# Kernel tuning notes

Hardware: AMD Instinct MI355X
Metric: run time of the kernel (lower is better)

Reference implementation:

```python
import jax, jax.numpy as jnp
import numpy as np

N, E, G = 50000, 500000, 1024
ND, ED, H, L, OUT = 32, 16, 128, 4, 1
BN_EPS = 1e-5


def setup_inputs() -> dict:
    key = jax.random.key(0)
    ks = jax.random.split(key, 32)

    def w(k, shape, fan):
        return jax.random.normal(k, shape, jnp.float32) / np.float32(np.sqrt(fan))

    inp = {
        "x": jax.random.normal(ks[0], (N, ND), jnp.float32),
        "edge_index": jax.random.randint(ks[1], (2, E), 0, N, jnp.int64),
        "edge_attr": jax.random.normal(ks[2], (E, ED), jnp.float32),
        "batch": jax.random.randint(ks[3], (N,), 0, G, jnp.int64),
        # embeddings
        "ne_w": w(ks[4], (ND, H), ND), "ne_b": jnp.zeros((H,), jnp.float32),
        "ee_w": w(ks[5], (ED, H), ED), "ee_b": jnp.zeros((H,), jnp.float32),
        # per-layer node_mlp: Linear(2H,H) ReLU Linear(H,H) BN(H)
        "nm_w1": w(ks[6], (L, 2 * H, H), 2 * H), "nm_b1": jnp.zeros((L, H), jnp.float32),
        "nm_w2": w(ks[7], (L, H, H), H), "nm_b2": jnp.zeros((L, H), jnp.float32),
        "bn_g": jnp.ones((L, H), jnp.float32), "bn_b": jnp.zeros((L, H), jnp.float32),
        # per-layer edge_mlp: Linear(H,H) ReLU Linear(H,H)  (edge_dim==hidden_dim inside MPNN)
        "em_w1": w(ks[8], (L, H, H), H), "em_b1": jnp.zeros((L, H), jnp.float32),
        "em_w2": w(ks[9], (L, H, H), H), "em_b2": jnp.zeros((L, H), jnp.float32),
        # readout: Linear(H,H) ReLU Dropout(eval=identity) Linear(H,OUT)
        "ro_w1": w(ks[10], (H, H), H), "ro_b1": jnp.zeros((H,), jnp.float32),
        "ro_w2": w(ks[11], (H, OUT), H), "ro_b2": jnp.zeros((OUT,), jnp.float32),
    }
    return inp


def reference(x, edge_index, edge_attr, batch,
              ne_w, ne_b, ee_w, ee_b,
              nm_w1, nm_b1, nm_w2, nm_b2, bn_g, bn_b,
              em_w1, em_b1, em_w2, em_b2,
              ro_w1, ro_b1, ro_w2, ro_b2):
    src, dst = edge_index[0], edge_index[1]  # PyG default: x_j from source, aggregate at target
    h = x @ ne_w + ne_b                      # [N, H]
    e = edge_attr @ ee_w + ee_b              # [E, H]
    inv_std = np.float32(1.0 / np.sqrt(1.0 + BN_EPS))  # eval BN, running_mean=0, running_var=1
    for l in range(nm_w1.shape[0]):
        # edge_mlp
        e = jax.nn.relu(e @ em_w1[l] + em_b1[l]) @ em_w2[l] + em_b2[l]
        # message: concat(x_j, edge_attr) -> node_mlp
        msg = jnp.concatenate([h[src], e], axis=1)              # [E, 2H]
        msg = jax.nn.relu(msg @ nm_w1[l] + nm_b1[l]) @ nm_w2[l] + nm_b2[l]
        msg = msg * (inv_std * bn_g[l]) + bn_b[l]               # BatchNorm1d (eval)
        # scatter-add aggregation + residual update
        agg = jax.ops.segment_sum(msg, dst, num_segments=h.shape[0])
        h = agg + h
    pooled = jax.ops.segment_sum(h, batch, num_segments=G)      # global_add_pool -> [G, H]
    return jax.nn.relu(pooled @ ro_w1 + ro_b1) @ ro_w2 + ro_b2  # [G, OUT]
```

## Files before the change

### kernel.cpp

```cpp
#include <hip/hip_runtime.h>
#include <hip/hip_bf16.h>
#include <math.h>

#define NN 50000
#define EE 500000
#define GG 1024
#define NDIM 32
#define EDIM 16
#define HH 128
#define LL 4
#define NT2 ((EE + 127) / 128)
#define NB2 ((NN + 127) / 128)
#define SCAN_NB ((NN + 255) / 256)

typedef unsigned short ushortT;
typedef __attribute__((ext_vector_type(8))) short bf16x8;
typedef __attribute__((ext_vector_type(4))) float f32x4;

#define MFMA16(a, b, c) __builtin_amdgcn_mfma_f32_16x16x32_bf16(a, b, c, 0, 0, 0)

__device__ inline float bf2f(ushortT u) {
    union { unsigned int i; float f; } v; v.i = ((unsigned int)u) << 16; return v.f;
}
__device__ inline ushortT f2bf(float f) {
    union { float f; unsigned int i; } v; v.f = f;
    unsigned int r = v.i + 0x7FFFu + ((v.i >> 16) & 1u);
    return (ushortT)(r >> 16);
}
__device__ inline short f2bfs(float f) { return (short)f2bf(f); }

__device__ inline bf16x8 lds_a(const char* base, int strideB, int row, int colByte,
                               int mask) {
    int b = row * strideB + colByte;
    b ^= ((row & mask) << 4);
    return *reinterpret_cast<const bf16x8*>(base + b);
}

__global__ __launch_bounds__(256) void hist_kernel(
        const int* __restrict__ dst, int* __restrict__ counts) {
    int i = blockIdx.x * 256 + threadIdx.x;
    if (i < EE) atomicAdd(&counts[dst[i]], 1);
}

__global__ __launch_bounds__(256) void scan_part1(
        const int* __restrict__ counts, int* __restrict__ bsum) {
    __shared__ int buf[256];
    int t = threadIdx.x;
    int i = blockIdx.x * 256 + t;
    buf[t] = (i < NN) ? counts[i] : 0;
    __syncthreads();
    for (int s = 128; s > 0; s >>= 1) {
        if (t < s) buf[t] += buf[t + s];
        __syncthreads();
    }
    if (t == 0) bsum[blockIdx.x] = buf[0];
}

__global__ __launch_bounds__(256) void scan_part2(
        const int* __restrict__ bsum, int* __restrict__ bbase) {
    __shared__ int buf[256];
    int t = threadIdx.x;
    int v = (t < SCAN_NB) ? bsum[t] : 0;
    buf[t] = v;
    __syncthreads();
    for (int off = 1; off < 256; off <<= 1) {
        int s = (t >= off) ? buf[t - off] : 0;
        __syncthreads();
        buf[t] += s;
        __syncthreads();
    }
    if (t < SCAN_NB) bbase[t] = buf[t] - v;
}

__global__ __launch_bounds__(256) void scan_part3(
        const int* __restrict__ counts, const int* __restrict__ bbase,
        int* __restrict__ base) {
    __shared__ int buf[256];
    int t = threadIdx.x;
    int i = blockIdx.x * 256 + t;
    int v = (i < NN) ? counts[i] : 0;
    buf[t] = v;
    __syncthreads();
    for (int off = 1; off < 256; off <<= 1) {
        int s = (t >= off) ? buf[t - off] : 0;
        __syncthreads();
        buf[t] += s;
        __syncthreads();
    }
    if (i < NN) base[i] = bbase[blockIdx.x] + buf[t] - v;
}

__global__ __launch_bounds__(256) void build_perm_kernel(
        const int* __restrict__ src, const int* __restrict__ dst,
        const int* __restrict__ base, int* __restrict__ cnt,
        int* __restrict__ perm, int* __restrict__ srcS, int* __restrict__ dstS) {
    int i = blockIdx.x * 256 + threadIdx.x;
    if (i >= EE) return;
    int d = dst[i];
    int pos = base[d] + atomicAdd(&cnt[d], 1);
    perm[pos] = i;
    srcS[pos] = src[i];
    dstS[pos] = d;
}

__global__ __launch_bounds__(256) void transpose_kernel(
        const float* __restrict__ in, ushortT* __restrict__ out, int K, int N) {
    int per = K * N;
    int total = LL * per;
    int idx = blockIdx.x * 256 + threadIdx.x;
    if (idx >= total) return;
    int l = idx / per, rem = idx - l * per;
    int n = rem / K, k = rem - n * K;
    out[idx] = f2bf(in[(size_t)l * per + (size_t)k * N + n]);
}

__global__ __launch_bounds__(256) void transpose_ee_kernel(
        const float* __restrict__ in, ushortT* __restrict__ out) {
    int idx = blockIdx.x * 256 + threadIdx.x;
    if (idx >= HH * 32) return;
    int n = idx >> 5, k = idx & 31;
    out[idx] = (k < EDIM) ? f2bf(in[k * HH + n]) : (ushortT)0;
}

__global__ __launch_bounds__(256) void bnfold_kernel(
        const float* __restrict__ w2, const float* __restrict__ b2,
        const float* __restrict__ bng, const float* __restrict__ bnb,
        ushortT* __restrict__ w2g, float* __restrict__ nb2g, float inv_std) {
    int idx = blockIdx.x * 256 + threadIdx.x;
    if (idx < LL * HH * HH) {
        int l = idx / (HH * HH), rem = idx - l * (HH * HH);
        int n = rem / HH, k = rem - n * HH;
        w2g[idx] = f2bf(w2[(size_t)l * HH * HH + (size_t)k * HH + n] *
                        bng[l * HH + n] * inv_std);
    }
    if (idx < LL * HH) {
        nb2g[idx] = b2[idx] * bng[idx] * inv_std + bnb[idx];
    }
}

__global__ __launch_bounds__(128) void node_embed_kernel(
        const float* __restrict__ x, const float* __restrict__ w,
        const float* __restrict__ b, float* __restrict__ h) {
    __shared__ float xs[NDIM];
    int i = blockIdx.x, j = threadIdx.x;
    if (j < NDIM) xs[j] = x[(size_t)i * NDIM + j];
    __syncthreads();
    float acc = b[j];
#pragma unroll
    for (int k = 0; k < NDIM; ++k) acc += xs[k] * w[k * HH + j];
    h[(size_t)i * HH + j] = acc;
}

template<int K, int KS, bool HASB>
__device__ inline void gemm_b(const char* aBase, int aStrideB, int aMask,
        const ushortT* __restrict__ wT, const float* __restrict__ bias,
        int wr, int wc, int l15, int lg, f32x4 acc[2][4]) {
#pragma unroll
    for (int ntl = 0; ntl < 4; ++ntl) {
        float bb = HASB ? bias[wc * 64 + ntl * 16 + l15] : 0.f;
        f32x4 iv = {bb, bb, bb, bb};
        acc[0][ntl] = iv;
        acc[1][ntl] = iv;
    }
#pragma unroll
    for (int ks = 0; ks < K / 32; ++ks) {
        int kk = ks * 32 + lg * 8;
        bf16x8 a0 = lds_a(aBase, aStrideB, wr * 32 + l15,      kk * 2, aMask);
        bf16x8 a1 = lds_a(aBase, aStrideB, wr * 32 + 16 + l15, kk * 2, aMask);
#pragma unroll
        for (int ntl = 0; ntl < 4; ++ntl) {
            int n = wc * 64 + ntl * 16 + l15;
            bf16x8 b = *reinterpret_cast<const bf16x8*>(wT + (size_t)n * KS + kk);
            acc[0][ntl] = MFMA16(a0, b, acc[0][ntl]);
            acc[1][ntl] = MFMA16(a1, b, acc[1][ntl]);
        }
    }
}

__device__ inline void gemm_uinit3(const char* aBase, const char* uBase,
        const ushortT* __restrict__ wT,
        int wr, int wc, int l15, int lg, f32x4 acc[2][4]) {
#pragma unroll
    for (int mt = 0; mt < 2; ++mt)
#pragma unroll
        for (int ntl = 0; ntl < 4; ++ntl) {
            int col = wc * 64 + ntl * 16 + l15;
#pragma unroll
            for (int r = 0; r < 4; ++r) {
                int row = wr * 32 + mt * 16 + lg * 4 + r;
                int b = row * 256 + col * 2; b ^= ((row & 7) << 4);
                acc[mt][ntl][r] = bf2f(*reinterpret_cast<const ushortT*>(uBase + b));
            }
        }
#pragma unroll
    for (int ks = 0; ks < 4; ++ks) {
        int kk = ks * 32 + lg * 8;
        bf16x8 a0 = lds_a(aBase, 256, wr * 32 + l15,      kk * 2, 7);
        bf16x8 a1 = lds_a(aBase, 256, wr * 32 + 16 + l15, kk * 2, 7);
#pragma unroll
        for (int ntl = 0; ntl < 4; ++ntl) {
            int n = wc * 64 + ntl * 16 + l15;
            bf16x8 b = *reinterpret_cast<const bf16x8*>(wT + (size_t)n * 256 + kk);
            acc[0][ntl] = MFMA16(a0, b, acc[0][ntl]);
            acc[1][ntl] = MFMA16(a1, b, acc[1][ntl]);
        }
    }
}

__device__ inline void wfrag(char* base, int wr, int wc, int l15, int lg,
                             f32x4 acc[2][4], bool relu) {
#pragma unroll
    for (int mt = 0; mt < 2; ++mt)
#pragma unroll
        for (int ntl = 0; ntl < 4; ++ntl) {
            int col = wc * 64 + ntl * 16 + l15;
#pragma unroll
            for (int r = 0; r < 4; ++r) {
                int row = wr * 32 + mt * 16 + lg * 4 + r;
                int b = row * 256 + col * 2;
                b ^= ((row & 7) << 4);
                float v = acc[mt][ntl][r];
                if (relu) v = fmaxf(v, 0.f);
                *reinterpret_cast<ushortT*>(base + b) = f2bf(v);
            }
        }
}

template<int EMBED, int LASTL>
__global__ __launch_bounds__(512) void edgeA_kernel(
        const ushortT* __restrict__ u, ushortT* __restrict__ e,
        const int* __restrict__ srcS, const int* __restrict__ dstS,
        const int* __restrict__ basep, const int* __restrict__ perm,
        const float* __restrict__ ea,
        const ushortT* __restrict__ eewT, const float* __restrict__ eeb,
        const ushortT* __restrict__ ew1t, const float* __restrict__ eb1,
        const ushortT* __restrict__ ew2t, const float* __restrict__ eb2,
        const ushortT* __restrict__ nw1bt,
        ushortT* __restrict__ partials) {
    __shared__ __align__(16) char eT[128 * 256];
    __shared__ __align__(16) char uT[128 * 256];
    __shared__ int dstx[128], bstartL[128], sidx[128], pidx[128];

    const int e0 = blockIdx.x * 128;
    int V = EE - e0; if (V > 128) V = 128;
    const int tid = threadIdx.x;
    const bf16x8 z8 = {0, 0, 0, 0, 0, 0, 0, 0};

    if (tid < 128) {
        int ii = e0 + tid;
        int d = (ii < EE) ? dstS[ii] : -1;
        dstx[tid] = d;
        bstartL[tid] = (d >= 0) ? basep[d] : 0;
        sidx[tid] = (ii < EE) ? srcS[ii] : 0;
        if (EMBED) pidx[tid] = (ii < EE) ? perm[ii] : 0;
    }
    __syncthreads();

#pragma unroll
    for (int s = 0; s < 4; ++s) {
        int idx = tid + s * 512;
        int row = idx >> 4, c8 = (idx & 15) * 8;
        bf16x8 v = *reinterpret_cast<const bf16x8*>(u + (size_t)sidx[row] * HH + c8);
        int b = row * 256 + c8 * 2; b ^= ((row & 7) << 4);
        *reinterpret_cast<bf16x8*>(uT + b) = v;
    }
    if (EMBED) {
        {
            int row = tid >> 2, q4 = (tid & 3) * 4;
            float4 v = *reinterpret_cast<const float4*>(
                ea + (size_t)pidx[row] * EDIM + q4);
            unsigned long long pack =
                (unsigned long long)f2bf(v.x) |
                ((unsigned long long)f2bf(v.y) << 16) |
                ((unsigned long long)f2bf(v.z) << 32) |
                ((unsigned long long)f2bf(v.w) << 48);
            int b = row * 64 + q4 * 2; b ^= ((row & 3) << 4);
            *reinterpret_cast<unsigned long long*>(eT + b) = pack;
        }
        if (tid < 256) {
            int row = tid >> 1;
            int b = row * 64 + 32 + (tid & 1) * 16; b ^= ((row & 3) << 4);
            *reinterpret_cast<bf16x8*>(eT + b) = z8;
        }
    } else {
#pragma unroll
        for (int s = 0; s < 4; ++s) {
            int idx = tid + s * 512;
            int row = idx >> 4, c8 = (idx & 15) * 8;
            bf16x8 v = *reinterpret_cast<const bf16x8*>(
                e + (size_t)(e0 + row) * HH + c8);
            int b = row * 256 + c8 * 2; b ^= ((row & 7) << 4);
            *reinterpret_cast<bf16x8*>(eT + b) = v;
        }
    }
    __syncthreads();

    const int wid = tid >> 6, lane = tid & 63;
    const int wr = wid >> 1, wc = wid & 1, l15 = lane & 15, lg = lane >> 4;
    f32x4 acc[2][4];

    if (EMBED) {
        gemm_b<32, 32, true>(eT, 64, 3, eewT, eeb, wr, wc, l15, lg, acc);
        __syncthreads();
        wfrag(eT, wr, wc, l15, lg, acc, false);
        __syncthreads();
    }
    gemm_b<HH, HH, true>(eT, 256, 7, ew1t, eb1, wr, wc, l15, lg, acc);
    __syncthreads();
    wfrag(eT, wr, wc, l15, lg, acc, true);
    __syncthreads();
    gemm_b<HH, HH, true>(eT, 256, 7, ew2t, eb2, wr, wc, l15, lg, acc);
    __syncthreads();
    wfrag(eT, wr, wc, l15, lg, acc, false);
    __syncthreads();
    if (!LASTL) {
#pragma unroll
        for (int s = 0; s < 4; ++s) {
            int idx = tid + s * 512;
            int row = idx >> 4, c8 = (idx & 15) * 8;
            if (row < V) {
                int b = row * 256 + c8 * 2; b ^= ((row & 7) << 4);
                *reinterpret_cast<bf16x8*>(e + (size_t)(e0 + row) * HH + c8) =
                    *reinterpret_cast<const bf16x8*>(eT + b);
            }
        }
    }
    gemm_uinit3(eT, uT, nw1bt, wr, wc, l15, lg, acc);
    __syncthreads();
    wfrag(eT, wr, wc, l15, lg, acc, true);
    __syncthreads();

    {
        int col = tid & 127, seg = tid >> 7;
        int r = seg * 32, rend = r + 32;
        float sum = 0.f;
        int dprev = -1, runStart = r;
        for (; r < rend; ++r) {
            int d = dstx[r];
            if (d != dprev) {
                if (dprev >= 0) {
                    int slot = ((e0 + runStart) >> 5) - (bstartL[runStart] >> 5);
                    if (slot < 3)
                        partials[((size_t)slot * NN + dprev) * HH + col] = f2bf(sum);
                }
                sum = 0.f; dprev = d; runStart = r;
            }
            if (d >= 0) {
                int b = r * 256 + col * 2; b ^= ((r & 7) << 4);
                sum += bf2f(*reinterpret_cast<const ushortT*>(eT + b));
            }
        }
        if (dprev >= 0) {
            int slot = ((e0 + runStart) >> 5) - (bstartL[runStart] >> 5);
            if (slot < 3)
                partials[((size_t)slot * NN + dprev) * HH + col] = f2bf(sum);
        }
    }
}

template<int HASU>
__global__ __launch_bounds__(512) void nodeB_kernel(
        const ushortT* __restrict__ partials, const int* __restrict__ basep,
        const ushortT* __restrict__ w2g, const float* __restrict__ nb2g,
        float* __restrict__ h,
        const ushortT* __restrict__ w1tn, const float* __restrict__ b1n,
        ushortT* __restrict__ uOut) {
    __shared__ __align__(16) char sT[128 * 256];
    __shared__ int degx[128];
    const int n0 = blockIdx.x * 128;
    int V = NN - n0; if (V > 128) V = 128;
    const int tid = threadIdx.x;

    __shared__ int basex[128];
    if (tid < 128) {
        int bs = 0, de = 0;
        if (tid < V) {
            int n = n0 + tid;
            bs = basep[n];
            int be = (n + 1 < NN) ? basep[n + 1] : EE;
            de = be - bs;
        }
        basex[tid] = bs;
        degx[tid] = de;
    }
    __syncthreads();

#pragma unroll
    for (int g = 0; g < 4; ++g) {
        int node = g * 32 + (tid >> 4);
        int c8 = (tid & 15) * 8;
        float s[8] = {0.f, 0.f, 0.f, 0.f, 0.f, 0.f, 0.f, 0.f};
        if (node < V) {
            int bs = basex[node], de = degx[node];
            if (de > 0) {
                int ns = ((bs + de - 1) >> 5) - (bs >> 5) + 1;
                if (ns > 3) ns = 3;
                for (int sl = 0; sl < ns; ++sl) {
                    bf16x8 pv = *reinterpret_cast<const bf16x8*>(
                        partials + ((size_t)sl * NN + n0 + node) * HH + c8);
#pragma unroll
                    for (int j = 0; j < 8; ++j) s[j] += bf2f((ushortT)pv[j]);
                }
            }
        }
        bf16x8 o;
#pragma unroll
        for (int j = 0; j < 8; ++j) o[j] = f2bfs(s[j]);
        int b = node * 256 + c8 * 2; b ^= ((node & 7) << 4);
        *reinterpret_cast<bf16x8*>(sT + b) = o;
    }
    __syncthreads();

    const int wid = tid >> 6, lane = tid & 63;
    const int wr = wid >> 1, wc = wid & 1, l15 = lane & 15, lg = lane >> 4;
    f32x4 acc[2][4];

    gemm_b<HH, HH, false>(sT, 256, 7, w2g, nullptr, wr, wc, l15, lg, acc);
#pragma unroll
    for (int ntl = 0; ntl < 4; ++ntl) {
        int col = wc * 64 + ntl * 16 + l15;
        float bg = nb2g[col];
#pragma unroll
        for (int mt = 0; mt < 2; ++mt)
#pragma unroll
            for (int r = 0; r < 4; ++r) {
                int row = wr * 32 + mt * 16 + lg * 4 + r;
                if (row < V) {
                    size_t off = (size_t)(n0 + row) * HH + col;
                    float hn = h[off] + acc[mt][ntl][r] + (float)degx[row] * bg;
                    h[off] = hn;
                    acc[mt][ntl][r] = hn;
                } else {
                    acc[mt][ntl][r] = 0.f;
                }
            }
    }
    if (HASU) {
        __syncthreads();
        wfrag(sT, wr, wc, l15, lg, acc, false);
        __syncthreads();
        gemm_b<HH, 2 * HH, true>(sT, 256, 7, w1tn, b1n, wr, wc, l15, lg, acc);
        __syncthreads();
        wfrag(sT, wr, wc, l15, lg, acc, false);
        __syncthreads();
#pragma unroll
        for (int s = 0; s < 4; ++s) {
            int idx = tid + s * 512;
            int row = idx >> 4, c8 = (idx & 15) * 8;
            if (row < V) {
                int b = row * 256 + c8 * 2; b ^= ((row & 7) << 4);
                *reinterpret_cast<bf16x8*>(uOut + (size_t)(n0 + row) * HH + c8) =
                    *reinterpret_cast<const bf16x8*>(sT + b);
            }
        }
    }
}

__global__ __launch_bounds__(512) void node_pre_kernel(
        const float* __restrict__ h, const ushortT* __restrict__ w1t,
        const float* __restrict__ b1, ushortT* __restrict__ uo) {
    __shared__ __align__(16) char sT[128 * 256];
    const int n0 = blockIdx.x * 128;
    int V = NN - n0; if (V > 128) V = 128;
    const int tid = threadIdx.x;
#pragma unroll
    for (int s = 0; s < 4; ++s) {
        int idx = tid + s * 512;
        int row = idx >> 4, c8 = (idx & 15) * 8;
        bf16x8 o = {0, 0, 0, 0, 0, 0, 0, 0};
        if (row < V) {
            const float* hp = h + (size_t)(n0 + row) * HH + c8;
            float4 va = *reinterpret_cast<const float4*>(hp);
            float4 vb = *reinterpret_cast<const float4*>(hp + 4);
            o[0] = f2bfs(va.x); o[1] = f2bfs(va.y); o[2] = f2bfs(va.z); o[3] = f2bfs(va.w);
            o[4] = f2bfs(vb.x); o[5] = f2bfs(vb.y); o[6] = f2bfs(vb.z); o[7] = f2bfs(vb.w);
        }
        int b = row * 256 + c8 * 2; b ^= ((row & 7) << 4);
        *reinterpret_cast<bf16x8*>(sT + b) = o;
    }
    __syncthreads();
    const int wid = tid >> 6, lane = tid & 63;
    const int wr = wid >> 1, wc = wid & 1, l15 = lane & 15, lg = lane >> 4;
    f32x4 acc[2][4];
    gemm_b<HH, 2 * HH, true>(sT, 256, 7, w1t, b1, wr, wc, l15, lg, acc);
    __syncthreads();
    wfrag(sT, wr, wc, l15, lg, acc, false);
    __syncthreads();
#pragma unroll
    for (int s = 0; s < 4; ++s) {
        int idx = tid + s * 512;
        int row = idx >> 4, c8 = (idx & 15) * 8;
        if (row < V) {
            int b = row * 256 + c8 * 2; b ^= ((row & 7) << 4);
            *reinterpret_cast<bf16x8*>(uo + (size_t)(n0 + row) * HH + c8) =
                *reinterpret_cast<const bf16x8*>(sT + b);
        }
    }
}

__global__ __launch_bounds__(256) void pool_kernel(
        const float* __restrict__ h, const int* __restrict__ batch,
        float* __restrict__ pooled) {
    long long idx = (long long)blockIdx.x * 256 + threadIdx.x;
    if (idx >= (long long)NN * HH) return;
    int i = (int)(idx >> 7), c = (int)(idx & 127);
    atomicAdd(&pooled[(size_t)batch[i] * HH + c], h[idx]);
}

__global__ __launch_bounds__(128) void readout_kernel(
        const float* __restrict__ pooled,
        const float* __restrict__ w1, const float* __restrict__ b1,
        const float* __restrict__ w2, const float* __restrict__ b2,
        float* __restrict__ out) {
    __shared__ float row[HH];
    __shared__ float red[HH];
    int g = blockIdx.x, j = threadIdx.x;
    row[j] = pooled[(size_t)g * HH + j];
    __syncthreads();
    float acc = b1[j];
    for (int k = 0; k < HH; ++k) acc += row[k] * w1[k * HH + j];
    red[j] = fmaxf(acc, 0.f) * w2[j];
    __syncthreads();
    for (int s = 64; s > 0; s >>= 1) {
        if (j < s) red[j] += red[j + s];
        __syncthreads();
    }
    if (j == 0) out[g] = red[0] + b2[0];
}

extern "C" void kernel_launch(void* const* d_in, const int* in_sizes, int n_in,
                              void* d_out, int out_size, void* d_ws, size_t ws_size,
                              hipStream_t stream) {
    const float* x     = (const float*)d_in[0];
    const int*   ei    = (const int*)d_in[1];
    const float* ea    = (const float*)d_in[2];
    const int*   batch = (const int*)d_in[3];
    const float* ne_w  = (const float*)d_in[4];
    const float* ne_b  = (const float*)d_in[5];
    const float* ee_w  = (const float*)d_in[6];
    const float* ee_b  = (const float*)d_in[7];
    const float* nm_w1 = (const float*)d_in[8];
    const float* nm_b1 = (const float*)d_in[9];
    const float* nm_w2 = (const float*)d_in[10];
    const float* nm_b2 = (const float*)d_in[11];
    const float* bn_g  = (const float*)d_in[12];
    const float* bn_b  = (const float*)d_in[13];
    const float* em_w1 = (const float*)d_in[14];
    const float* em_b1 = (const float*)d_in[15];
    const float* em_w2 = (const float*)d_in[16];
    const float* em_b2 = (const float*)d_in[17];
    const float* ro_w1 = (const float*)d_in[18];
    const float* ro_b1 = (const float*)d_in[19];
    const float* ro_w2 = (const float*)d_in[20];
    const float* ro_b2 = (const float*)d_in[21];

    const int* srcp = ei;
    const int* dstp = ei + EE;

    char* p = (char*)d_ws;
    float* h = (float*)p;            p += (size_t)NN * HH * 4;
    float* pooled = (float*)p;       p += (size_t)GG * HH * 4;
    ushortT* ebuf = (ushortT*)p;     p += (size_t)EE * HH * 2;
    ushortT* ubuf = (ushortT*)p;     p += (size_t)NN * HH * 2;
    ushortT* partials = (ushortT*)p; p += (size_t)3 * NN * HH * 2;
    ushortT* ew1t = (ushortT*)p;     p += (size_t)LL * HH * HH * 2;
    ushortT* ew2t = (ushortT*)p;     p += (size_t)LL * HH * HH * 2;
    ushortT* nw1t = (ushortT*)p;     p += (size_t)LL * 2 * HH * HH * 2;
    ushortT* w2g  = (ushortT*)p;     p += (size_t)LL * HH * HH * 2;
    float* nb2g   = (float*)p;       p += (size_t)LL * HH * 4;
    ushortT* eewT = (ushortT*)p;     p += (size_t)HH * 32 * 2;
    int* perm   = (int*)p;           p += (size_t)EE * 4;
    int* srcS   = (int*)p;           p += (size_t)EE * 4;
    int* dstS   = (int*)p;           p += (size_t)EE * 4;
    int* counts = (int*)p;           p += (size_t)NN * 4;
    int* basep  = (int*)p;           p += (size_t)NN * 4;
    int* cnt    = (int*)p;           p += (size_t)NN * 4;
    int* bsum   = (int*)p;           p += (size_t)SCAN_NB * 4;
    int* bbase  = (int*)p;           p += (size_t)SCAN_NB * 4;

    hipMemsetAsync(counts, 0, (size_t)NN * 4, stream);
    hipMemsetAsync(cnt, 0, (size_t)NN * 4, stream);
    hist_kernel<<<(EE + 255) / 256, 256, 0, stream>>>(dstp, counts);
    scan_part1<<<SCAN_NB, 256, 0, stream>>>(counts, bsum);
    scan_part2<<<1, 256, 0, stream>>>(bsum, bbase);
    scan_part3<<<SCAN_NB, 256, 0, stream>>>(counts, bbase, basep);
    build_perm_kernel<<<(EE + 255) / 256, 256, 0, stream>>>(
        srcp, dstp, basep, cnt, perm, srcS, dstS);

    const float inv_std = 1.0f / sqrtf(1.0f + 1e-5f);
    transpose_kernel<<<(LL * HH * HH + 255) / 256, 256, 0, stream>>>(em_w1, ew1t, HH, HH);
    transpose_kernel<<<(LL * HH * HH + 255) / 256, 256, 0, stream>>>(em_w2, ew2t, HH, HH);
    transpose_kernel<<<(LL * 2 * HH * HH + 255) / 256, 256, 0, stream>>>(nm_w1, nw1t, 2 * HH, HH);
    bnfold_kernel<<<(LL * HH * HH + 255) / 256, 256, 0, stream>>>(
        nm_w2, nm_b2, bn_g, bn_b, w2g, nb2g, inv_std);
    transpose_ee_kernel<<<(HH * 32 + 255) / 256, 256, 0, stream>>>(ee_w, eewT);

    node_embed_kernel<<<NN, 128, 0, stream>>>(x, ne_w, ne_b, h);
    node_pre_kernel<<<NB2, 512, 0, stream>>>(h, nw1t, nm_b1, ubuf);

    for (int l = 0; l < LL; ++l) {
        const ushortT* nw1bt = nw1t + (size_t)l * 2 * HH * HH + 128;
        if (l == 0) {
            edgeA_kernel<1, 0><<<NT2, 512, 0, stream>>>(
                ubuf, ebuf, srcS, dstS, basep, perm, ea, eewT, ee_b,
                ew1t + (size_t)l * HH * HH, em_b1 + l * HH,
                ew2t + (size_t)l * HH * HH, em_b2 + l * HH,
                nw1bt, partials);
        } else if (l < LL - 1) {
            edgeA_kernel<0, 0><<<NT2, 512, 0, stream>>>(
                ubuf, ebuf, srcS, dstS, basep, perm, ea, eewT, ee_b,
                ew1t + (size_t)l * HH * HH, em_b1 + l * HH,
                ew2t + (size_t)l * HH * HH, em_b2 + l * HH,
                nw1bt, partials);
        } else {
            edgeA_kernel<0, 1><<<NT2, 512, 0, stream>>>(
                ubuf, ebuf, srcS, dstS, basep, perm, ea, eewT, ee_b,
                ew1t + (size_t)l * HH * HH, em_b1 + l * HH,
                ew2t + (size_t)l * HH * HH, em_b2 + l * HH,
                nw1bt, partials);
        }
        if (l < LL - 1) {
            nodeB_kernel<1><<<NB2, 512, 0, stream>>>(
                partials, basep, w2g + (size_t)l * HH * HH, nb2g + l * HH, h,
                nw1t + (size_t)(l + 1) * 2 * HH * HH, nm_b1 + (l + 1) * HH, ubuf);
        } else {
            nodeB_kernel<0><<<NB2, 512, 0, stream>>>(
                partials, basep, w2g + (size_t)l * HH * HH, nb2g + l * HH, h,
                nw1t, nm_b1, ubuf);
        }
    }

    hipMemsetAsync(pooled, 0, sizeof(float) * (size_t)GG * HH, stream);
    {
        long long total = (long long)NN * HH;
        pool_kernel<<<(int)((total + 255) / 256), 256, 0, stream>>>(h, batch, pooled);
    }
    readout_kernel<<<GG, 128, 0, stream>>>(pooled, ro_w1, ro_b1, ro_w2, ro_b2,
                                           (float*)d_out);
}
```

Measured before the change: 1.196 ms.

## Fuse node embedding into MFMA pre-kernel, sort pooling by graph, trim edge kernel LDS

The scalar per-node embedding kernel is replaced by an MFMA GEMM fused into the node pre-kernel, which writes h and the projected u in one pass. Global add pooling now builds a per-graph permutation with a histogram, scan and scatter, and does segmented reduction per graph instead of 6.4M float atomics. The edge kernel prefetches the gathered source rows into registers rather than a second LDS tile, and reuses two LDS buffers in ping-pong fashion to cut barriers and shared memory. Together these add preprocessing launches and register pressure.

```diff
diff --git a/kernel.cpp b/kernel.cpp
--- a/kernel.cpp
+++ b/kernel.cpp
@@ -9,7 +9,7 @@
 #define EDIM 16
 #define HH 128
 #define LL 4
-#define NT2 ((EE + 127) / 128)
+#define NT128 ((EE + 127) / 128)
 #define NB2 ((NN + 127) / 128)
 #define SCAN_NB ((NN + 255) / 256)
 
@@ -103,6 +103,38 @@
     dstS[pos] = d;
 }
 
+__global__ __launch_bounds__(256) void ghist_kernel(
+        const int* __restrict__ batch, int* __restrict__ gcounts) {
+    int i = blockIdx.x * 256 + threadIdx.x;
+    if (i < NN) atomicAdd(&gcounts[batch[i]], 1);
+}
+
+__global__ __launch_bounds__(1024) void gscan_kernel(
+        const int* __restrict__ gcounts, int* __restrict__ gbase) {
+    __shared__ int buf[1024];
+    int t = threadIdx.x;
+    int v = gcounts[t];
+    buf[t] = v;
+    __syncthreads();
+    for (int off = 1; off < 1024; off <<= 1) {
+        int s = (t >= off) ? buf[t - off] : 0;
+        __syncthreads();
+        buf[t] += s;
+        __syncthreads();
+    }
+    gbase[t] = buf[t] - v;
+}
+
+__global__ __launch_bounds__(256) void gbuild_kernel(
+        const int* __restrict__ batch, const int* __restrict__ gbase,
+        int* __restrict__ gcnt, int* __restrict__ gperm) {
+    int i = blockIdx.x * 256 + threadIdx.x;
+    if (i >= NN) return;
+    int b = batch[i];
+    int pos = gbase[b] + atomicAdd(&gcnt[b], 1);
+    gperm[pos] = i;
+}
+
 __global__ __launch_bounds__(256) void transpose_kernel(
         const float* __restrict__ in, ushortT* __restrict__ out, int K, int N) {
     int per = K * N;
@@ -114,12 +146,12 @@
     out[idx] = f2bf(in[(size_t)l * per + (size_t)k * N + n]);
 }
 
-__global__ __launch_bounds__(256) void transpose_ee_kernel(
-        const float* __restrict__ in, ushortT* __restrict__ out) {
+__global__ __launch_bounds__(256) void transpose_pad32_kernel(
+        const float* __restrict__ in, ushortT* __restrict__ out, int KIN) {
     int idx = blockIdx.x * 256 + threadIdx.x;
     if (idx >= HH * 32) return;
     int n = idx >> 5, k = idx & 31;
-    out[idx] = (k < EDIM) ? f2bf(in[k * HH + n]) : (ushortT)0;
+    out[idx] = (k < KIN) ? f2bf(in[k * HH + n]) : (ushortT)0;
 }
 
 __global__ __launch_bounds__(256) void bnfold_kernel(
@@ -138,19 +170,6 @@
     }
 }
 
-__global__ __launch_bounds__(128) void node_embed_kernel(
-        const float* __restrict__ x, const float* __restrict__ w,
-        const float* __restrict__ b, float* __restrict__ h) {
-    __shared__ float xs[NDIM];
-    int i = blockIdx.x, j = threadIdx.x;
-    if (j < NDIM) xs[j] = x[(size_t)i * NDIM + j];
-    __syncthreads();
-    float acc = b[j];
-#pragma unroll
-    for (int k = 0; k < NDIM; ++k) acc += xs[k] * w[k * HH + j];
-    h[(size_t)i * HH + j] = acc;
-}
-
 template<int K, int KS, bool HASB>
 __device__ inline void gemm_b(const char* aBase, int aStrideB, int aMask,
         const ushortT* __restrict__ wT, const float* __restrict__ bias,
@@ -171,36 +190,6 @@
         for (int ntl = 0; ntl < 4; ++ntl) {
             int n = wc * 64 + ntl * 16 + l15;
             bf16x8 b = *reinterpret_cast<const bf16x8*>(wT + (size_t)n * KS + kk);
-            acc[0][ntl] = MFMA16(a0, b, acc[0][ntl]);
-            acc[1][ntl] = MFMA16(a1, b, acc[1][ntl]);
-        }
-    }
-}
-
-__device__ inline void gemm_uinit3(const char* aBase, const char* uBase,
-        const ushortT* __restrict__ wT,
-        int wr, int wc, int l15, int lg, f32x4 acc[2][4]) {
-#pragma unroll
-    for (int mt = 0; mt < 2; ++mt)
-#pragma unroll
-        for (int ntl = 0; ntl < 4; ++ntl) {
-            int col = wc * 64 + ntl * 16 + l15;
-#pragma unroll
-            for (int r = 0; r < 4; ++r) {
-                int row = wr * 32 + mt * 16 + lg * 4 + r;
-                int b = row * 256 + col * 2; b ^= ((row & 7) << 4);
-                acc[mt][ntl][r] = bf2f(*reinterpret_cast<const ushortT*>(uBase + b));
-            }
-        }
-#pragma unroll
-    for (int ks = 0; ks < 4; ++ks) {
-        int kk = ks * 32 + lg * 8;
-        bf16x8 a0 = lds_a(aBase, 256, wr * 32 + l15,      kk * 2, 7);
-        bf16x8 a1 = lds_a(aBase, 256, wr * 32 + 16 + l15, kk * 2, 7);
-#pragma unroll
-        for (int ntl = 0; ntl < 4; ++ntl) {
-            int n = wc * 64 + ntl * 16 + l15;
-            bf16x8 b = *reinterpret_cast<const bf16x8*>(wT + (size_t)n * 256 + kk);
             acc[0][ntl] = MFMA16(a0, b, acc[0][ntl]);
             acc[1][ntl] = MFMA16(a1, b, acc[1][ntl]);
         }
@@ -238,80 +227,76 @@
         const ushortT* __restrict__ nw1bt,
         ushortT* __restrict__ partials) {
     __shared__ __align__(16) char eT[128 * 256];
-    __shared__ __align__(16) char uT[128 * 256];
-    __shared__ int dstx[128], bstartL[128], sidx[128], pidx[128];
+    __shared__ __align__(16) char hidM[128 * 256];
+    __shared__ int dstx[128], bstartL[128];
 
     const int e0 = blockIdx.x * 128;
     int V = EE - e0; if (V > 128) V = 128;
     const int tid = threadIdx.x;
+    const int wid = tid >> 6, lane = tid & 63;
+    const int wr = wid >> 1, wc = wid & 1, l15 = lane & 15, lg = lane >> 4;
     const bf16x8 z8 = {0, 0, 0, 0, 0, 0, 0, 0};
+
+    bf16x8 ureg[4];
+#pragma unroll
+    for (int s = 0; s < 4; ++s) {
+        int idx = tid + s * 512;
+        int row = idx >> 4, c8 = (idx & 15) * 8;
+        int g = e0 + row;
+        int sI = (g < EE) ? srcS[g] : 0;
+        ureg[s] = *reinterpret_cast<const bf16x8*>(u + (size_t)sI * HH + c8);
+    }
 
     if (tid < 128) {
         int ii = e0 + tid;
         int d = (ii < EE) ? dstS[ii] : -1;
         dstx[tid] = d;
         bstartL[tid] = (d >= 0) ? basep[d] : 0;
-        sidx[tid] = (ii < EE) ? srcS[ii] : 0;
-        if (EMBED) pidx[tid] = (ii < EE) ? perm[ii] : 0;
-    }
-    __syncthreads();
-
-#pragma unroll
-    for (int s = 0; s < 4; ++s) {
-        int idx = tid + s * 512;
-        int row = idx >> 4, c8 = (idx & 15) * 8;
-        bf16x8 v = *reinterpret_cast<const bf16x8*>(u + (size_t)sidx[row] * HH + c8);
-        int b = row * 256 + c8 * 2; b ^= ((row & 7) << 4);
-        *reinterpret_cast<bf16x8*>(uT + b) = v;
-    }
+    }
+
     if (EMBED) {
-        {
-            int row = tid >> 2, q4 = (tid & 3) * 4;
-            float4 v = *reinterpret_cast<const float4*>(
-                ea + (size_t)pidx[row] * EDIM + q4);
-            unsigned long long pack =
-                (unsigned long long)f2bf(v.x) |
-                ((unsigned long long)f2bf(v.y) << 16) |
-                ((unsigned long long)f2bf(v.z) << 32) |
-                ((unsigned long long)f2bf(v.w) << 48);
-            int b = row * 64 + q4 * 2; b ^= ((row & 3) << 4);
-            *reinterpret_cast<unsigned long long*>(eT + b) = pack;
-        }
+        int row = tid >> 2, q4 = (tid & 3) * 4;
+        unsigned long long pack = 0ull;
+        if (row < V) {
+            int pp = perm[e0 + row];
+            float4 v = *reinterpret_cast<const float4*>(ea + (size_t)pp * EDIM + q4);
+            pack = (unsigned long long)f2bf(v.x) |
+                   ((unsigned long long)f2bf(v.y) << 16) |
+                   ((unsigned long long)f2bf(v.z) << 32) |
+                   ((unsigned long long)f2bf(v.w) << 48);
+        }
+        int b = row * 64 + q4 * 2; b ^= ((row & 3) << 4);
+        *reinterpret_cast<unsigned long long*>(eT + b) = pack;
         if (tid < 256) {
-            int row = tid >> 1;
-            int b = row * 64 + 32 + (tid & 1) * 16; b ^= ((row & 3) << 4);
-            *reinterpret_cast<bf16x8*>(eT + b) = z8;
+            int prow = tid >> 1;
+            int bb = prow * 64 + 32 + (tid & 1) * 16; bb ^= ((prow & 3) << 4);
+            *reinterpret_cast<bf16x8*>(eT + bb) = z8;
         }
     } else {
 #pragma unroll
         for (int s = 0; s < 4; ++s) {
             int idx = tid + s * 512;
             int row = idx >> 4, c8 = (idx & 15) * 8;
-            bf16x8 v = *reinterpret_cast<const bf16x8*>(
-                e + (size_t)(e0 + row) * HH + c8);
+            bf16x8 v = z8;
+            if (row < V)
+                v = *reinterpret_cast<const bf16x8*>(e + (size_t)(e0 + row) * HH + c8);
             int b = row * 256 + c8 * 2; b ^= ((row & 7) << 4);
-            *reinterpret_cast<bf16x8*>(eT + b) = v;
-        }
-    }
-    __syncthreads();
-
-    const int wid = tid >> 6, lane = tid & 63;
-    const int wr = wid >> 1, wc = wid & 1, l15 = lane & 15, lg = lane >> 4;
+            *reinterpret_cast<bf16x8*>(hidM + b) = v;
+        }
+    }
+    __syncthreads();
+
     f32x4 acc[2][4];
-
     if (EMBED) {
         gemm_b<32, 32, true>(eT, 64, 3, eewT, eeb, wr, wc, l15, lg, acc);
-        __syncthreads();
-        wfrag(eT, wr, wc, l15, lg, acc, false);
-        __syncthreads();
-    }
-    gemm_b<HH, HH, true>(eT, 256, 7, ew1t, eb1, wr, wc, l15, lg, acc);
-    __syncthreads();
+        wfrag(hidM, wr, wc, l15, lg, acc, false);
+        __syncthreads();
+    }
+    gemm_b<HH, HH, true>(hidM, 256, 7, ew1t, eb1, wr, wc, l15, lg, acc);
     wfrag(eT, wr, wc, l15, lg, acc, true);
     __syncthreads();
     gemm_b<HH, HH, true>(eT, 256, 7, ew2t, eb2, wr, wc, l15, lg, acc);
-    __syncthreads();
-    wfrag(eT, wr, wc, l15, lg, acc, false);
+    wfrag(hidM, wr, wc, l15, lg, acc, false);
     __syncthreads();
     if (!LASTL) {
 #pragma unroll
@@ -321,11 +306,42 @@
             if (row < V) {
                 int b = row * 256 + c8 * 2; b ^= ((row & 7) << 4);
                 *reinterpret_cast<bf16x8*>(e + (size_t)(e0 + row) * HH + c8) =
-                    *reinterpret_cast<const bf16x8*>(eT + b);
-            }
-        }
-    }
-    gemm_uinit3(eT, uT, nw1bt, wr, wc, l15, lg, acc);
+                    *reinterpret_cast<const bf16x8*>(hidM + b);
+            }
+        }
+    }
+#pragma unroll
+    for (int s = 0; s < 4; ++s) {
+        int idx = tid + s * 512;
+        int row = idx >> 4, c8 = (idx & 15) * 8;
+        int b = row * 256 + c8 * 2; b ^= ((row & 7) << 4);
+        *reinterpret_cast<bf16x8*>(eT + b) = ureg[s];
+    }
+    __syncthreads();
+#pragma unroll
+    for (int mt = 0; mt < 2; ++mt)
+#pragma unroll
+        for (int ntl = 0; ntl < 4; ++ntl)
+#pragma unroll
+            for (int r = 0; r < 4; ++r) {
+                int row = wr * 32 + mt * 16 + lg * 4 + r;
+                int col = wc * 64 + ntl * 16 + l15;
+                int b = row * 256 + col * 2; b ^= ((row & 7) << 4);
+                acc[mt][ntl][r] = bf2f(*reinterpret_cast<const ushortT*>(eT + b));
+            }
+#pragma unroll
+    for (int ks = 0; ks < 4; ++ks) {
+        int kk = ks * 32 + lg * 8;
+        bf16x8 a0 = lds_a(hidM, 256, wr * 32 + l15,      kk * 2, 7);
+        bf16x8 a1 = lds_a(hidM, 256, wr * 32 + 16 + l15, kk * 2, 7);
+#pragma unroll
+        for (int ntl = 0; ntl < 4; ++ntl) {
+            int n = wc * 64 + ntl * 16 + l15;
+            bf16x8 b = *reinterpret_cast<const bf16x8*>(nw1bt + (size_t)n * 256 + kk);
+            acc[0][ntl] = MFMA16(a0, b, acc[0][ntl]);
+            acc[1][ntl] = MFMA16(a1, b, acc[1][ntl]);
+        }
+    }
     __syncthreads();
     wfrag(eT, wr, wc, l15, lg, acc, true);
     __syncthreads();
@@ -367,11 +383,11 @@
         ushortT* __restrict__ uOut) {
     __shared__ __align__(16) char sT[128 * 256];
     __shared__ int degx[128];
+    __shared__ int basex[128];
     const int n0 = blockIdx.x * 128;
     int V = NN - n0; if (V > 128) V = 128;
     const int tid = threadIdx.x;
 
-    __shared__ int basex[128];
     if (tid < 128) {
         int bs = 0, de = 0;
         if (tid < V) {
@@ -456,32 +472,53 @@
     }
 }
 
-__global__ __launch_bounds__(512) void node_pre_kernel(
-        const float* __restrict__ h, const ushortT* __restrict__ w1t,
-        const float* __restrict__ b1, ushortT* __restrict__ uo) {
+__global__ __launch_bounds__(512) void node_pre2_kernel(
+        const float* __restrict__ x, const ushortT* __restrict__ newT,
+        const float* __restrict__ neb,
+        const ushortT* __restrict__ w1t, const float* __restrict__ b1,
+        float* __restrict__ h, ushortT* __restrict__ uo) {
     __shared__ __align__(16) char sT[128 * 256];
+    __shared__ __align__(16) char xT[128 * 64];
     const int n0 = blockIdx.x * 128;
     int V = NN - n0; if (V > 128) V = 128;
     const int tid = threadIdx.x;
-#pragma unroll
-    for (int s = 0; s < 4; ++s) {
+
+#pragma unroll
+    for (int s = 0; s < 2; ++s) {
         int idx = tid + s * 512;
-        int row = idx >> 4, c8 = (idx & 15) * 8;
-        bf16x8 o = {0, 0, 0, 0, 0, 0, 0, 0};
+        int row = idx >> 3;
+        int q4 = (idx & 7) * 4;
+        unsigned long long pack = 0ull;
         if (row < V) {
-            const float* hp = h + (size_t)(n0 + row) * HH + c8;
-            float4 va = *reinterpret_cast<const float4*>(hp);
-            float4 vb = *reinterpret_cast<const float4*>(hp + 4);
-            o[0] = f2bfs(va.x); o[1] = f2bfs(va.y); o[2] = f2bfs(va.z); o[3] = f2bfs(va.w);
-            o[4] = f2bfs(vb.x); o[5] = f2bfs(vb.y); o[6] = f2bfs(vb.z); o[7] = f2bfs(vb.w);
-        }
-        int b = row * 256 + c8 * 2; b ^= ((row & 7) << 4);
-        *reinterpret_cast<bf16x8*>(sT + b) = o;
-    }
-    __syncthreads();
+            float4 v = *reinterpret_cast<const float4*>(
+                x + (size_t)(n0 + row) * NDIM + q4);
+            pack = (unsigned long long)f2bf(v.x) |
+                   ((unsigned long long)f2bf(v.y) << 16) |
+                   ((unsigned long long)f2bf(v.z) << 32) |
+                   ((unsigned long long)f2bf(v.w) << 48);
+        }
+        int b = row * 64 + q4 * 2; b ^= ((row & 3) << 4);
+        *reinterpret_cast<unsigned long long*>(xT + b) = pack;
+    }
+    __syncthreads();
+
     const int wid = tid >> 6, lane = tid & 63;
     const int wr = wid >> 1, wc = wid & 1, l15 = lane & 15, lg = lane >> 4;
     f32x4 acc[2][4];
+    gemm_b<32, 32, true>(xT, 64, 3, newT, neb, wr, wc, l15, lg, acc);
+#pragma unroll
+    for (int mt = 0; mt < 2; ++mt)
+#pragma unroll
+        for (int ntl = 0; ntl < 4; ++ntl) {
+            int col = wc * 64 + ntl * 16 + l15;
+#pragma unroll
+            for (int r = 0; r < 4; ++r) {
+                int row = wr * 32 + mt * 16 + lg * 4 + r;
+                if (row < V) h[(size_t)(n0 + row) * HH + col] = acc[mt][ntl][r];
+            }
+        }
+    wfrag(sT, wr, wc, l15, lg, acc, false);
+    __syncthreads();
     gemm_b<HH, 2 * HH, true>(sT, 256, 7, w1t, b1, wr, wc, l15, lg, acc);
     __syncthreads();
     wfrag(sT, wr, wc, l15, lg, acc, false);
@@ -498,13 +535,22 @@
     }
 }
 
-__global__ __launch_bounds__(256) void pool_kernel(
-        const float* __restrict__ h, const int* __restrict__ batch,
+__global__ __launch_bounds__(256) void pool2_kernel(
+        const float* __restrict__ h, const int* __restrict__ gperm,
+        const int* __restrict__ gbase, const int* __restrict__ gcounts,
         float* __restrict__ pooled) {
-    long long idx = (long long)blockIdx.x * 256 + threadIdx.x;
-    if (idx >= (long long)NN * HH) return;
-    int i = (int)(idx >> 7), c = (int)(idx & 127);
-    atomicAdd(&pooled[(size_t)batch[i] * HH + c], h[idx]);
+    int w = threadIdx.x >> 6, lane = threadIdx.x & 63;
+    int g = blockIdx.x * 4 + w;
+    int bs = gbase[g], cnt = gcounts[g];
+    int c = lane * 2;
+    float ax = 0.f, ay = 0.f;
+    for (int j = 0; j < cnt; ++j) {
+        int n = gperm[bs + j];
+        float2 v = *reinterpret_cast<const float2*>(h + (size_t)n * HH + c);
+        ax += v.x; ay += v.y;
+    }
+    float2 o = {ax, ay};
+    *reinterpret_cast<float2*>(pooled + (size_t)g * HH + c) = o;
 }
 
 __global__ __launch_bounds__(128) void readout_kernel(
@@ -569,6 +615,7 @@
     ushortT* w2g  = (ushortT*)p;     p += (size_t)LL * HH * HH * 2;
     float* nb2g   = (float*)p;       p += (size_t)LL * HH * 4;
     ushortT* eewT = (ushortT*)p;     p += (size_t)HH * 32 * 2;
+    ushortT* newT = (ushortT*)p;     p += (size_t)HH * 32 * 2;
     int* perm   = (int*)p;           p += (size_t)EE * 4;
     int* srcS   = (int*)p;           p += (size_t)EE * 4;
     int* dstS   = (int*)p;           p += (size_t)EE * 4;
@@ -577,9 +624,15 @@
     int* cnt    = (int*)p;           p += (size_t)NN * 4;
     int* bsum   = (int*)p;           p += (size_t)SCAN_NB * 4;
     int* bbase  = (int*)p;           p += (size_t)SCAN_NB * 4;
+    int* gperm  = (int*)p;           p += (size_t)NN * 4;
+    int* gcounts= (int*)p;           p += (size_t)GG * 4;
+    int* gbase  = (int*)p;           p += (size_t)GG * 4;
+    int* gcnt   = (int*)p;           p += (size_t)GG * 4;
 
     hipMemsetAsync(counts, 0, (size_t)NN * 4, stream);
     hipMemsetAsync(cnt, 0, (size_t)NN * 4, stream);
+    hipMemsetAsync(gcounts, 0, (size_t)GG * 4, stream);
+    hipMemsetAsync(gcnt, 0, (size_t)GG * 4, stream);
     hist_kernel<<<(EE + 255) / 256, 256, 0, stream>>>(dstp, counts);
     scan_part1<<<SCAN_NB, 256, 0, stream>>>(counts, bsum);
     scan_part2<<<1, 256, 0, stream>>>(bsum, bbase);
@@ -587,33 +640,37 @@
     build_perm_kernel<<<(EE + 255) / 256, 256, 0, stream>>>(
         srcp, dstp, basep, cnt, perm, srcS, dstS);
 
+    ghist_kernel<<<(NN + 255) / 256, 256, 0, stream>>>(batch, gcounts);
+    gscan_kernel<<<1, 1024, 0, stream>>>(gcounts, gbase);
+    gbuild_kernel<<<(NN + 255) / 256, 256, 0, stream>>>(batch, gbase, gcnt, gperm);
+
     const float inv_std = 1.0f / sqrtf(1.0f + 1e-5f);
     transpose_kernel<<<(LL * HH * HH + 255) / 256, 256, 0, stream>>>(em_w1, ew1t, HH, HH);
     transpose_kernel<<<(LL * HH * HH + 255) / 256, 256, 0, stream>>>(em_w2, ew2t, HH, HH);
     transpose_kernel<<<(LL * 2 * HH * HH + 255) / 256, 256, 0, stream>>>(nm_w1, nw1t, 2 * HH, HH);
     bnfold_kernel<<<(LL * HH * HH + 255) / 256, 256, 0, stream>>>(
         nm_w2, nm_b2, bn_g, bn_b, w2g, nb2g, inv_std);
-    transpose_ee_kernel<<<(HH * 32 + 255) / 256, 256, 0, stream>>>(ee_w, eewT);
-
-    node_embed_kernel<<<NN, 128, 0, stream>>>(x, ne_w, ne_b, h);
-    node_pre_kernel<<<NB2, 512, 0, stream>>>(h, nw1t, nm_b1, ubuf);
+    transpose_pad32_kernel<<<(HH * 32 + 255) / 256, 256, 0, stream>>>(ee_w, eewT, EDIM);
+    transpose_pad32_kernel<<<(HH * 32 + 255) / 256, 256, 0, stream>>>(ne_w, newT, NDIM);
+
+    node_pre2_kernel<<<NB2, 512, 0, stream>>>(x, newT, ne_b, nw1t, nm_b1, h, ubuf);
 
     for (int l = 0; l < LL; ++l) {
         const ushortT* nw1bt = nw1t + (size_t)l * 2 * HH * HH + 128;
         if (l == 0) {
-            edgeA_kernel<1, 0><<<NT2, 512, 0, stream>>>(
+            edgeA_kernel<1, 0><<<NT128, 512, 0, stream>>>(
                 ubuf, ebuf, srcS, dstS, basep, perm, ea, eewT, ee_b,
                 ew1t + (size_t)l * HH * HH, em_b1 + l * HH,
                 ew2t + (size_t)l * HH * HH, em_b2 + l * HH,
                 nw1bt, partials);
         } else if (l < LL - 1) {
-            edgeA_kernel<0, 0><<<NT2, 512, 0, stream>>>(
+            edgeA_kernel<0, 0><<<NT128, 512, 0, stream>>>(
                 ubuf, ebuf, srcS, dstS, basep, perm, ea, eewT, ee_b,
                 ew1t + (size_t)l * HH * HH, em_b1 + l * HH,
                 ew2t + (size_t)l * HH * HH, em_b2 + l * HH,
                 nw1bt, partials);
         } else {
-            edgeA_kernel<0, 1><<<NT2, 512, 0, stream>>>(
+            edgeA_kernel<0, 1><<<NT128, 512, 0, stream>>>(
                 ubuf, ebuf, srcS, dstS, basep, perm, ea, eewT, ee_b,
                 ew1t + (size_t)l * HH * HH, em_b1 + l * HH,
                 ew2t + (size_t)l * HH * HH, em_b2 + l * HH,
@@ -630,11 +687,7 @@
         }
     }
 
-    hipMemsetAsync(pooled, 0, sizeof(float) * (size_t)GG * HH, stream);
-    {
-        long long total = (long long)NN * HH;
-        pool_kernel<<<(int)((total + 255) / 256), 256, 0, stream>>>(h, batch, pooled);
-    }
+    pool2_kernel<<<GG / 4, 256, 0, stream>>>(h, gperm, gbase, gcounts, pooled);
     readout_kernel<<<GG, 128, 0, stream>>>(pooled, ro_w1, ro_b1, ro_w2, ro_b2,
                                            (float*)d_out);
 }
```

Measured after the change: 1.645 ms. 1.38x slower.
